# Kernel tuning notes

Hardware: AMD Instinct MI355X
Metric: run time of the kernel (lower is better)

The kernel has to match this reference:

```python
import jax, jax.numpy as jnp
import numpy as np

NPOINT = 1024
BRANCHES = [(0.4, 32), (0.8, 64)]  # (radius, nsample)
SPECS = [[67, 64, 64, 128], [67, 64, 128, 256]]  # mlp specs after use_xyz (+3)
EPS = 1e-5


def setup_inputs() -> dict:
    key = jax.random.key(0)
    ks = jax.random.split(key, 16)
    B, N, C = 8, 8192, 64
    inp = {
        "xyz": jax.random.normal(ks[0], (B, N, 3), jnp.float32),
        "features": jax.random.normal(ks[1], (B, C, N), jnp.float32),
    }
    ki = 2
    for bi, spec in enumerate(SPECS):
        for li in range(3):
            o, i = spec[li + 1], spec[li]
            inp[f"w{bi}_{li}"] = jax.random.normal(ks[ki], (o, i), jnp.float32) * (1.0 / np.sqrt(i)); ki += 1
            inp[f"g{bi}_{li}"] = jnp.ones((o,), jnp.float32)
            inp[f"b{bi}_{li}"] = jnp.zeros((o,), jnp.float32)
    return inp


def fps(pts, npoint):
    # pts: [B, N+1, 3] (mean point prepended); sequential farthest point sampling
    B, N1, _ = pts.shape

    def step(carry, _):
        dist, far = carry
        idx3 = jnp.broadcast_to(far[:, None, None], (B, 1, 3))
        centroid = jnp.take_along_axis(pts, idx3, axis=1)  # [B,1,3]
        d = jnp.sum((pts - centroid) ** 2, axis=-1)        # [B,N+1]
        dist = jnp.minimum(dist, d)
        far2 = jnp.argmax(dist, axis=-1)
        return (dist, far2), centroid[:, 0, :]

    dist0 = jnp.full((B, N1), 1e10, jnp.float32)
    far0 = jnp.zeros((B,), jnp.int32)
    _, locs = jax.lax.scan(step, (dist0, far0), None, length=npoint)
    return jnp.transpose(locs, (1, 0, 2))  # [B, npoint, 3]


def ball_query(xyz, new_xyz, radius, nsample):
    # first <=nsample indices with dist^2 < radius^2, padded with first valid (0 if none)
    B, N, _ = xyz.shape
    d2 = jnp.sum((new_xyz[:, :, None, :] - xyz[:, None, :, :]) ** 2, axis=-1)  # [B,S,N]
    score = jnp.where(d2 < radius * radius, jnp.arange(N, dtype=jnp.int32), N)
    vals, _ = jax.lax.top_k(-score, nsample)  # smallest scores = earliest valid indices
    idx = -vals                               # [B,S,nsample], N marks invalid
    first = idx[..., :1]
    first = jnp.where(first < N, first, 0)
    return jnp.where(idx < N, idx, first)


def _forward(xyz, features, params):
    mean = jnp.mean(xyz, axis=1, keepdims=True)
    pts = jnp.concatenate([mean, xyz], axis=1)          # prepend mean point
    new_xyz = jax.lax.stop_gradient(fps(pts, NPOINT))   # [B,npoint,3] (torch no_grad)
    outs = []
    for (radius, nsample), layers in zip(BRANCHES, params):
        idx = ball_query(xyz, new_xyz, radius, nsample)           # [B,S,K]
        gxyz = jax.vmap(lambda p, i: p[i])(xyz, idx)              # [B,S,K,3]
        rel = jnp.transpose(gxyz - new_xyz[:, :, None, :], (0, 3, 1, 2))  # [B,3,S,K]
        gfeat = jax.vmap(lambda f, i: f[:, i])(features, idx)     # [B,C,S,K]
        x = jnp.concatenate([rel, gfeat], axis=1)                 # [B,3+C,S,K]
        for W, g, b in layers:  # Conv2d 1x1 (no bias) + BatchNorm (train stats) + ReLU
            x = jnp.einsum('oi,bisk->bosk', W, x)
            m = jnp.mean(x, axis=(0, 2, 3), keepdims=True)
            v = jnp.var(x, axis=(0, 2, 3), keepdims=True)
            x = (x - m) / jnp.sqrt(v + EPS) * g[None, :, None, None] + b[None, :, None, None]
            x = jax.nn.relu(x)
        outs.append(jnp.max(x, axis=3))                           # [B,Cout,S]
    return new_xyz, jnp.concatenate(outs, axis=1)


def reference(xyz, features,
              w0_0, g0_0, b0_0, w0_1, g0_1, b0_1, w0_2, g0_2, b0_2,
              w1_0, g1_0, b1_0, w1_1, g1_1, b1_1, w1_2, g1_2, b1_2):
    params = [
        [(w0_0, g0_0, b0_0), (w0_1, g0_1, b0_1), (w0_2, g0_2, b0_2)],
        [(w1_0, g1_0, b1_0), (w1_1, g1_1, b1_1), (w1_2, g1_2, b1_2)],
    ]
    return _forward(xyz, features, params)
```

## Files before the change

kernel.cpp:

```cpp
#include <hip/hip_runtime.h>
#include <hip/hip_bf16.h>
#include <cstdint>


typedef __attribute__((ext_vector_type(8))) short short8;
typedef __attribute__((ext_vector_type(4))) float f32x4;
typedef __attribute__((ext_vector_type(2))) float f32x2;

__device__ __forceinline__ float bf2f(unsigned short u) {
    return __uint_as_float(((unsigned)u) << 16);
}
__device__ __forceinline__ unsigned short f2bf(float f) {
    unsigned u = __float_as_uint(f);
    return (unsigned short)((u + 0x7fffu + ((u >> 16) & 1u)) >> 16);
}

__device__ __forceinline__ float wave_red_max_f32(float v) {
#define DPPSTEP(ctrl)                                                                  \
    {                                                                                  \
        int _t = __builtin_amdgcn_update_dpp((int)0xFF800000, __float_as_int(v), ctrl, \
                                             0xf, 0xf, false);                         \
        v = fmaxf(v, __int_as_float(_t));                                              \
    }
    DPPSTEP(0x111) DPPSTEP(0x112) DPPSTEP(0x114) DPPSTEP(0x118) DPPSTEP(0x142) DPPSTEP(0x143)
#undef DPPSTEP
    return v;
}
__device__ __forceinline__ unsigned wave_red_min_u32(unsigned v) {
#define DPPSTEP(ctrl)                                                                   \
    {                                                                                   \
        unsigned _t = (unsigned)__builtin_amdgcn_update_dpp((int)0xFFFFFFFF, (int)v,    \
                                                            ctrl, 0xf, 0xf, false);     \
        v = v < _t ? v : _t;                                                            \
    }
    DPPSTEP(0x111) DPPSTEP(0x112) DPPSTEP(0x114) DPPSTEP(0x118) DPPSTEP(0x142) DPPSTEP(0x143)
#undef DPPSTEP
    return v;
}
__device__ __forceinline__ unsigned long long u64max(unsigned long long a, unsigned long long b) {
    return a > b ? a : b;
}
__device__ __forceinline__ unsigned u32min(unsigned a, unsigned b) { return a < b ? a : b; }

static const size_t OFF_WBF   = 0;
static const size_t OFF_STATS = 262144;
static const size_t STATS_BYTES = 720896;
static const size_t OFF_AFF   = 1048576;
static const size_t OFF_IDX0  = 2097152;
static const size_t OFF_IDX1  = 3145728;
static const size_t OFF_MX    = 5242880;
static const size_t OFF_MN    = 13631488;
static const size_t OFF_Y0    = 22020096;
static const size_t OFF_Y1    = 90177536;
static const size_t OFF_FEATT = 211812352;

__global__ __launch_bounds__(256) void fused_pre(
    const float* __restrict__ xyz, const float* __restrict__ feat,
    float* __restrict__ newxyz, unsigned short* __restrict__ ft,
    const float* __restrict__ w0, const float* __restrict__ w1, const float* __restrict__ w2,
    const float* __restrict__ w3, const float* __restrict__ w4, const float* __restrict__ w5,
    unsigned short* __restrict__ wb) {
    __shared__ union alignas(16) SM {
        struct {
            float ptsx[8200], ptsy[8200], ptsz[8200];
            float ldsM[16][3];
            float meanv[3];
            unsigned long long sKey[2][4];
            float cbuf[3072];
        } f;
        float tile[64][65];
    } sm;
    const int tid = threadIdx.x;

    if (blockIdx.x >= 1032) {
        int id = (int)(blockIdx.x - 1032) * 256 + tid;
        const int psz[6] = {6144, 4096, 8192, 6144, 8192, 32768};
        const int Kp[6] = {96, 64, 64, 96, 64, 128};
        const int Ks[6] = {67, 64, 64, 67, 64, 128};
        const float* wp[6] = {w0, w1, w2, w3, w4, w5};
        int off = 0;
        for (int l = 0; l < 6; ++l) {
            if (id < off + psz[l]) {
                int e = id - off;
                int m = e / Kp[l], k = e - m * Kp[l];
                float v = (k < Ks[l]) ? wp[l][m * Ks[l] + k] : 0.f;
                wb[id] = f2bf(v);
                return;
            }
            off += psz[l];
        }
        return;
    }

    if (blockIdx.x >= 8) {
        int tb = (int)blockIdx.x - 8;
        int b = tb >> 7;
        int j0 = (tb & 127) * 64;
#pragma unroll
        for (int i = 0; i < 16; ++i) {
            int e = i * 256 + tid;
            int c = e >> 6, j = e & 63;
            sm.tile[j][c] = feat[((size_t)b * 64 + c) * 8192 + j0 + j];
        }
        __syncthreads();
#pragma unroll
        for (int i = 0; i < 16; ++i) {
            int e = i * 256 + tid;
            int j = e >> 6, c = e & 63;
            ft[((size_t)(b * 8192 + j0 + j)) * 96 + 3 + c] = f2bf(sm.tile[j][c]);
        }
        if (tid < 64) {
            int j = tid;
            size_t base = ((size_t)(b * 8192 + j0 + j)) * 96;
            const float* xp = xyz + ((size_t)b * 8192 + j0 + j) * 3;
            ft[base + 0] = f2bf(xp[0]);
            ft[base + 1] = f2bf(xp[1]);
            ft[base + 2] = f2bf(xp[2]);
        } else if (tid < 128) {
            int j = tid - 64;
            size_t base = ((size_t)(b * 8192 + j0 + j)) * 96;
            for (int c = 67; c < 96; ++c) ft[base + c] = 0;
        }
        return;
    }

    const int b = blockIdx.x;
    const int t = tid;
    const int lane = t & 63, wv = t >> 6;
    const float* xb = xyz + (size_t)b * 8192 * 3;

    f32x2 px[16], py[16], pz[16], d[16];
#pragma unroll
    for (int k = 0; k < 16; ++k) {
        int q0 = t + 256 * (2 * k);
        int q1 = t + 256 * (2 * k + 1);
        px[k].x = xb[q0 * 3 + 0]; px[k].y = xb[q1 * 3 + 0];
        py[k].x = xb[q0 * 3 + 1]; py[k].y = xb[q1 * 3 + 1];
        pz[k].x = xb[q0 * 3 + 2]; pz[k].y = xb[q1 * 3 + 2];
        d[k].x = 1e10f; d[k].y = 1e10f;
        sm.f.ptsx[q0 + 1] = px[k].x; sm.f.ptsx[q1 + 1] = px[k].y;
        sm.f.ptsy[q0 + 1] = py[k].x; sm.f.ptsy[q1 + 1] = py[k].y;
        sm.f.ptsz[q0 + 1] = pz[k].x; sm.f.ptsz[q1 + 1] = pz[k].y;
    }
    {
        float sx[4], sy[4], sz[4];
#pragma unroll
        for (int m = 0; m < 4; ++m) {
            int u = (t + 256 * m + 1023) & 1023;
            float ax = 0.f, ay = 0.f, az = 0.f;
#pragma unroll
            for (int jj = 0; jj < 8; ++jj) {
                int ia = u + 1024 * jj;
                ax += xb[ia * 3 + 0]; ay += xb[ia * 3 + 1]; az += xb[ia * 3 + 2];
            }
            sx[m] = ax; sy[m] = ay; sz[m] = az;
        }
#pragma unroll
        for (int off = 32; off; off >>= 1) {
#pragma unroll
            for (int m = 0; m < 4; ++m) {
                sx[m] += __shfl_xor(sx[m], off, 64);
                sy[m] += __shfl_xor(sy[m], off, 64);
                sz[m] += __shfl_xor(sz[m], off, 64);
            }
        }
        if (lane == 0) {
#pragma unroll
            for (int m = 0; m < 4; ++m) {
                sm.f.ldsM[wv + 4 * m][0] = sx[m];
                sm.f.ldsM[wv + 4 * m][1] = sy[m];
                sm.f.ldsM[wv + 4 * m][2] = sz[m];
            }
        }
    }
    __syncthreads();
    if (t < 3) {
        float s = 0.f;
        for (int w = 0; w < 16; ++w) s += sm.f.ldsM[w][t];
        sm.f.meanv[t] = s * (1.f / 8192.f);
    }
    __syncthreads();
    float cx = sm.f.meanv[0], cy = sm.f.meanv[1], cz = sm.f.meanv[2];
    const float mmx = cx, mmy = cy, mmz = cz;
    float dm = 1e10f;
    if (t == 0) { sm.f.ptsx[0] = cx; sm.f.ptsy[0] = cy; sm.f.ptsz[0] = cz; }
    __syncthreads();

    for (int it = 0; it < 1024; ++it) {
        if (t == 0) {
            sm.f.cbuf[it * 3 + 0] = cx;
            sm.f.cbuf[it * 3 + 1] = cy;
            sm.f.cbuf[it * 3 + 2] = cz;
        }
        f32x2 c0, c1, c2, vm2;
        c0.x = cx; c0.y = cx; c1.x = cy; c1.y = cy; c2.x = cz; c2.y = cz;
        vm2.x = -1e30f; vm2.y = -1e30f;
        {
#pragma clang fp contract(off)
#pragma unroll
            for (int k = 0; k < 16; ++k) {
                f32x2 dx = px[k] - c0;
                f32x2 dy = py[k] - c1;
                f32x2 dz = pz[k] - c2;
                f32x2 dd = (dx * dx + dy * dy) + dz * dz;
                f32x2 nd = __builtin_elementwise_min(d[k], dd);
                d[k] = nd;
                vm2 = __builtin_elementwise_max(vm2, nd);
            }
        }
        float vmax = fmaxf(vm2.x, vm2.y);
        if (t == 0) {
            float dx = __fsub_rn(mmx, cx);
            float dy = __fsub_rn(mmy, cy);
            float dz = __fsub_rn(mmz, cz);
            float dd = __fadd_rn(__fadd_rn(__fmul_rn(dx, dx), __fmul_rn(dy, dy)), __fmul_rn(dz, dz));
            dm = fminf(dm, dd);
            vmax = fmaxf(vmax, dm);
        }
        float wm = wave_red_max_f32(vmax);
        float bmaxw = __int_as_float(__builtin_amdgcn_readlane(__float_as_int(wm), 63));
        unsigned m2[16];
#pragma unroll
        for (int k = 0; k < 16; ++k) {
            unsigned i0 = (d[k].x == bmaxw) ? (unsigned)(t + 256 * (2 * k) + 1) : 0xFFFFFFFFu;
            unsigned i1 = (d[k].y == bmaxw) ? (unsigned)(t + 256 * (2 * k + 1) + 1) : 0xFFFFFFFFu;
            m2[k] = u32min(i0, i1);
        }
#pragma unroll
        for (int s = 8; s; s >>= 1)
#pragma unroll
            for (int k = 0; k < s; ++k) m2[k] = u32min(m2[k], m2[k + s]);
        unsigned mi = m2[0];
        if (t == 0 && dm == bmaxw) mi = 0u;
        unsigned wmin = wave_red_min_u32(mi);
        unsigned miw = (unsigned)__builtin_amdgcn_readlane((int)wmin, 63);
        int par = it & 1;
        if (lane == 0)
            sm.f.sKey[par][wv] = ((unsigned long long)__float_as_uint(bmaxw) << 32) |
                                 (unsigned long long)(8192u - miw);
        __syncthreads();
        unsigned long long ka[4];
#pragma unroll
        for (int i = 0; i < 4; ++i) ka[i] = sm.f.sKey[par][i];
        unsigned long long kk = u64max(u64max(ka[0], ka[1]), u64max(ka[2], ka[3]));
        int far = 8192 - (int)(unsigned)(kk & 0xffffffffull);
        cx = sm.f.ptsx[far];
        cy = sm.f.ptsy[far];
        cz = sm.f.ptsz[far];
    }
    __syncthreads();
    float* ob = newxyz + (size_t)b * 3072;
#pragma unroll
    for (int i = 0; i < 12; ++i) ob[t + 256 * i] = sm.f.cbuf[t + 256 * i];
}

__global__ void ball_query2(const float* __restrict__ xyz, const float* __restrict__ newxyz,
                            int* __restrict__ idx0, int* __restrict__ idx1) {
    int bid = blockIdx.x;
    int br = (bid >= 2048);
    int K = br ? 64 : 32;
    float r2 = br ? (0.8f * 0.8f) : (0.4f * 0.4f);
    int* idxout = br ? idx1 : idx0;
    int wid = (((bid & 2047) * 256) + threadIdx.x) >> 6;
    int lane = threadIdx.x & 63;
    int b = wid >> 10;
    const float* q = newxyz + (size_t)wid * 3;
    float qx = q[0], qy = q[1], qz = q[2];
    const float* xb = xyz + (size_t)b * 8192 * 3;
    int* out = idxout + (size_t)wid * K;
    int count = 0;
    int first = 0;
    for (int base = 0; base < 8192 && count < K; base += 64) {
        int j = base + lane;
        float dx = __fsub_rn(xb[j * 3 + 0], qx);
        float dy = __fsub_rn(xb[j * 3 + 1], qy);
        float dz = __fsub_rn(xb[j * 3 + 2], qz);
        float d2 = __fadd_rn(__fadd_rn(__fmul_rn(dx, dx), __fmul_rn(dy, dy)), __fmul_rn(dz, dz));
        bool in = d2 < r2;
        unsigned long long m = __ballot(in);
        if (count == 0 && m) first = base + __ffsll((long long)m) - 1;
        if (in) {
            int pos = count + __popcll(m & ((1ull << lane) - 1ull));
            if (pos < K) out[pos] = j;
        }
        count += __popcll(m);
    }
    if (count < K) {
        int fillv = (count > 0) ? first : 0;
        for (int p = count + lane; p < K; p += 64) out[p] = fillv;
    }
}

template <int Mp, int Kp, int IN_MODE, int OUT_MODE, int KSH, int NT>
__global__ __launch_bounds__(256) void gemm_mfma(
    const unsigned short* __restrict__ Wb, const unsigned short* __restrict__ Xin,
    const float* __restrict__ aff, const int* __restrict__ idx,
    const unsigned short* __restrict__ ftp, const float* __restrict__ newxyz,
    unsigned short* __restrict__ Yout, float* __restrict__ MX, float* __restrict__ MN,
    float* __restrict__ statS, float* __restrict__ statQ) {
    constexpr int MT = Mp / 64;
    constexpr int KS = Kp / 32;
    constexpr int NC = NT * 16;
    constexpr int NCHUNK = NT * KS * 64;
    __shared__ unsigned short Bs[NCHUNK * 8];
    __shared__ float sAux[NT * 64];
    int* sAuxI = (int*)sAux;

    const int tid = threadIdx.x;
    const int w = tid >> 6;
    const int lane = tid & 63;
    const int n = lane & 15;
    const int quad = lane >> 4;
    const int rbase = w * (Mp / 4);
    const long col0 = (long)blockIdx.x * NC;

    short8 a[MT][KS];
#pragma unroll
    for (int mt = 0; mt < MT; ++mt)
#pragma unroll
        for (int ks = 0; ks < KS; ++ks)
            a[mt][ks] = *(const short8*)(Wb + (size_t)(rbase + mt * 16 + n) * Kp + ks * 32 + quad * 8);

    if constexpr (IN_MODE == 0) {
        for (int c = tid; c < NC; c += 256) {
            long colg = col0 + c;
            sAuxI[c] = idx[colg];
            long sk = colg >> KSH;
            sAux[NC + c] = newxyz[sk * 3 + 0];
            sAux[2 * NC + c] = newxyz[sk * 3 + 1];
            sAux[3 * NC + c] = newxyz[sk * 3 + 2];
        }
    } else {
        if (tid < 2 * Kp) sAux[tid] = aff[tid];
    }
    __syncthreads();

#pragma unroll
    for (int i = 0; i < NCHUNK / 256; ++i) {
        int p = i * 256 + tid;
        int pl = p & 63;
        int pn = pl & 15;
        int pq = pl >> 4;
        int rest = p >> 6;
        int pks = rest % KS;
        int pnt = rest / KS;
        int col = pnt * 16 + pn;
        int kc = pks * 4 + pq;
        short8 v;
        if constexpr (IN_MODE == 0) {
            const int bb = (int)(col0 >> (KSH + 10));
            int j = sAuxI[col];
            v = *(const short8*)(ftp + ((long)(bb * 8192 + j)) * 96 + kc * 8);
            if (kc == 0) {
                v[0] = (short)f2bf(bf2f((unsigned short)v[0]) - sAux[NC + col]);
                v[1] = (short)f2bf(bf2f((unsigned short)v[1]) - sAux[2 * NC + col]);
                v[2] = (short)f2bf(bf2f((unsigned short)v[2]) - sAux[3 * NC + col]);
            }
        } else {
            short8 raw = *(const short8*)(Xin + (col0 + col) * (long)Kp + kc * 8);
#pragma unroll
            for (int e = 0; e < 8; ++e) {
                float xf = bf2f((unsigned short)raw[e]);
                xf = fmaxf(fmaf(xf, sAux[kc * 8 + e], sAux[Kp + kc * 8 + e]), 0.f);
                v[e] = (short)f2bf(xf);
            }
        }
        *(short8*)(&Bs[p * 8]) = v;
    }
    __syncthreads();

    f32x4 acc[MT][NT];
#pragma unroll
    for (int mt = 0; mt < MT; ++mt)
#pragma unroll
        for (int nt = 0; nt < NT; ++nt)
#pragma unroll
            for (int r = 0; r < 4; ++r) acc[mt][nt][r] = 0.f;

#pragma unroll
    for (int ks = 0; ks < KS; ++ks) {
#pragma unroll
        for (int nt = 0; nt < NT; ++nt) {
            short8 bfr = *(const short8*)(&Bs[((nt * KS + ks) * 64 + lane) * 8]);
#pragma unroll
            for (int mt = 0; mt < MT; ++mt)
                acc[mt][nt] = __builtin_amdgcn_mfma_f32_16x16x32_bf16(a[mt][ks], bfr, acc[mt][nt], 0, 0, 0);
        }
    }

    const int slot = (int)(blockIdx.x & 127);
#pragma unroll
    for (int mt = 0; mt < MT; ++mt)
#pragma unroll
        for (int r = 0; r < 4; ++r) {
            float s = 0.f, q = 0.f;
#pragma unroll
            for (int nt = 0; nt < NT; ++nt) {
                float v = acc[mt][nt][r];
                s += v;
                q = fmaf(v, v, q);
            }
#pragma unroll
            for (int off = 1; off < 16; off <<= 1) {
                s += __shfl_xor(s, off, 16);
                q += __shfl_xor(q, off, 16);
            }
            if (n == 0) {
                int ch = rbase + mt * 16 + quad * 4 + r;
                atomicAdd(statS + (size_t)ch * 128 + slot, s);
                atomicAdd(statQ + (size_t)ch * 128 + slot, q);
            }
        }

    if constexpr (OUT_MODE == 0) {
#pragma unroll
        for (int mt = 0; mt < MT; ++mt)
#pragma unroll
            for (int nt = 0; nt < NT; ++nt) {
                long col = col0 + nt * 16 + n;
                unsigned p0 = f2bf(acc[mt][nt][0]) | ((unsigned)f2bf(acc[mt][nt][1]) << 16);
                unsigned p1 = f2bf(acc[mt][nt][2]) | ((unsigned)f2bf(acc[mt][nt][3]) << 16);
                uint2 st; st.x = p0; st.y = p1;
                *(uint2*)(Yout + col * Mp + rbase + mt * 16 + quad * 4) = st;
            }
    } else {
        constexpr int GRP = (1 << KSH) / 16;
        constexpr int NG = NT / GRP;
#pragma unroll
        for (int mt = 0; mt < MT; ++mt)
#pragma unroll
            for (int r = 0; r < 4; ++r) {
#pragma unroll
                for (int gh = 0; gh < NG; ++gh) {
                    float mx = acc[mt][GRP * gh][r], mn = acc[mt][GRP * gh][r];
#pragma unroll
                    for (int e = 1; e < GRP; ++e) {
                        mx = fmaxf(mx, acc[mt][GRP * gh + e][r]);
                        mn = fminf(mn, acc[mt][GRP * gh + e][r]);
                    }
#pragma unroll
                    for (int off = 1; off < 16; off <<= 1) {
                        mx = fmaxf(mx, __shfl_xor(mx, off, 16));
                        mn = fminf(mn, __shfl_xor(mn, off, 16));
                    }
                    if (n == 0) {
                        int ch = rbase + mt * 16 + quad * 4 + r;
                        long g = (col0 >> KSH) + gh;
                        MX[(long)ch * 8192 + g] = mx;
                        MN[(long)ch * 8192 + g] = mn;
                    }
                }
            }
    }
}

__global__ void finalize_kernel(const float* __restrict__ sS, const float* __restrict__ sQ,
                                const float* __restrict__ g, const float* __restrict__ b,
                                float* __restrict__ aff, int C, float invCount) {
    int c = threadIdx.x + blockIdx.x * blockDim.x;
    if (c >= C) return;
    float s = 0.f, q = 0.f;
    for (int k = 0; k < 128; ++k) { s += sS[c * 128 + k]; q += sQ[c * 128 + k]; }
    float mean = s * invCount;
    float var = fmaxf(q * invCount - mean * mean, 0.f);
    float sc = g[c] / sqrtf(var + 1e-5f);
    float sh = b[c] - mean * sc;
    aff[c] = sc;
    aff[C + c] = sh;
}

__global__ void final_out_kernel(const float* __restrict__ MX, const float* __restrict__ MN,
                                 const float* __restrict__ aff, float* __restrict__ out1,
                                 int Cout, int cOff) {
    long i = (long)blockIdx.x * 256 + threadIdx.x;
    int c = (int)(i >> 13);
    int gidx = (int)(i & 8191);
    int b = gidx >> 10, s = gidx & 1023;
    float sc = aff[c], sh = aff[Cout + c];
    float v = fmaxf(fmaxf(sc * MX[i] + sh, sc * MN[i] + sh), 0.f);
    out1[((long)b * 384 + cOff + c) * 1024 + s] = v;
}

extern "C" void kernel_launch(void* const* d_in, const int* in_sizes, int n_in,
                              void* d_out, int out_size, void* d_ws, size_t ws_size,
                              hipStream_t stream) {
    const float* xyz = (const float*)d_in[0];
    const float* feat = (const float*)d_in[1];
    const float *W[6], *G[6], *Bi[6];
    for (int l = 0; l < 6; ++l) {
        W[l] = (const float*)d_in[2 + l * 3];
        G[l] = (const float*)d_in[3 + l * 3];
        Bi[l] = (const float*)d_in[4 + l * 3];
    }
    char* ws = (char*)d_ws;
    float* out0 = (float*)d_out;
    float* out1 = (float*)d_out + 24576;

    unsigned short* wb = (unsigned short*)(ws + OFF_WBF);
    float* stats = (float*)(ws + OFF_STATS);
    float* affine = (float*)(ws + OFF_AFF);
    int* idx0 = (int*)(ws + OFF_IDX0);
    int* idx1 = (int*)(ws + OFF_IDX1);
    float* mx = (float*)(ws + OFF_MX);
    float* mn = (float*)(ws + OFF_MN);
    unsigned short* y0 = (unsigned short*)(ws + OFF_Y0);
    unsigned short* y1 = (unsigned short*)(ws + OFF_Y1);
    unsigned short* ftp = (unsigned short*)(ws + OFF_FEATT);

    hipMemsetAsync(stats, 0, STATS_BYTES, stream);
    fused_pre<<<1288, 256, 0, stream>>>(xyz, feat, out0, ftp, W[0], W[1], W[2], W[3], W[4],
                                        W[5], wb);
    ball_query2<<<4096, 256, 0, stream>>>(xyz, out0, idx0, idx1);

    const int wOff[6] = {0, 6144, 10240, 18432, 24576, 32768};
    int stOff[6], afOff[6];
    {
        const int Cs[6] = {64, 64, 128, 64, 128, 256};
        int so = 0, ao = 0;
        for (int l = 0; l < 6; ++l) {
            stOff[l] = so; so += Cs[l] * 256;
            afOff[l] = ao; ao += Cs[l] * 2;
        }
    }

    for (int br = 0; br < 2; ++br) {
        const int K = br ? 64 : 32;
        const long NCOL = 8L * 1024 * K;
        int* idx = br ? idx1 : idx0;
        const int l0 = br * 3, l1 = br * 3 + 1, l2 = br * 3 + 2;
        const int M2 = br ? 256 : 128;
        const float invCount = 1.f / (float)NCOL;
        const int nblk256 = (int)(NCOL / 256);
        const int nblk128 = (int)(NCOL / 128);
        const int nblk64 = (int)(NCOL / 64);

        if (br == 0) {
            gemm_mfma<64, 96, 0, 0, 5, 16><<<nblk256, 256, 0, stream>>>(
                wb + wOff[l0], nullptr, nullptr, idx, ftp, out0, y0, nullptr, nullptr,
                stats + stOff[l0], stats + stOff[l0] + 64 * 128);
            finalize_kernel<<<1, 256, 0, stream>>>(stats + stOff[l0], stats + stOff[l0] + 64 * 128,
                                                   G[l0], Bi[l0], affine + afOff[l0], 64, invCount);
            gemm_mfma<64, 64, 1, 0, 5, 16><<<nblk256, 256, 0, stream>>>(
                wb + wOff[l1], y0, affine + afOff[l0], nullptr, nullptr, nullptr, y1, nullptr,
                nullptr, stats + stOff[l1], stats + stOff[l1] + 64 * 128);
            finalize_kernel<<<1, 256, 0, stream>>>(stats + stOff[l1], stats + stOff[l1] + 64 * 128,
                                                   G[l1], Bi[l1], affine + afOff[l1], 64, invCount);
            gemm_mfma<128, 64, 1, 1, 5, 8><<<nblk128, 256, 0, stream>>>(
                wb + wOff[l2], y1, affine + afOff[l1], nullptr, nullptr, nullptr, nullptr, mx, mn,
                stats + stOff[l2], stats + stOff[l2] + 128 * 128);
            finalize_kernel<<<1, 256, 0, stream>>>(stats + stOff[l2], stats + stOff[l2] + 128 * 128,
                                                   G[l2], Bi[l2], affine + afOff[l2], 128, invCount);
        } else {
            gemm_mfma<64, 96, 0, 0, 6, 16><<<nblk256, 256, 0, stream>>>(
                wb + wOff[l0], nullptr, nullptr, idx, ftp, out0, y0, nullptr, nullptr,
                stats + stOff[l0], stats + stOff[l0] + 64 * 128);
            finalize_kernel<<<1, 256, 0, stream>>>(stats + stOff[l0], stats + stOff[l0] + 64 * 128,
                                                   G[l0], Bi[l0], affine + afOff[l0], 64, invCount);
            gemm_mfma<128, 64, 1, 0, 6, 8><<<nblk128, 256, 0, stream>>>(
                wb + wOff[l1], y0, affine + afOff[l0], nullptr, nullptr, nullptr, y1, nullptr,
                nullptr, stats + stOff[l1], stats + stOff[l1] + 128 * 128);
            finalize_kernel<<<1, 256, 0, stream>>>(stats + stOff[l1], stats + stOff[l1] + 128 * 128,
                                                   G[l1], Bi[l1], affine + afOff[l1], 128, invCount);
            gemm_mfma<256, 128, 1, 1, 6, 4><<<nblk64, 256, 0, stream>>>(
                wb + wOff[l2], y1, affine + afOff[l1], nullptr, nullptr, nullptr, nullptr, mx, mn,
                stats + stOff[l2], stats + stOff[l2] + 256 * 128);
            finalize_kernel<<<1, 256, 0, stream>>>(stats + stOff[l2], stats + stOff[l2] + 256 * 128,
                                                   G[l2], Bi[l2], affine + afOff[l2], 256, invCount);
        }

        final_out_kernel<<<(M2 * 8192) / 256, 256, 0, stream>>>(mx, mn, affine + afOff[l2], out1,
                                                                M2, br ? 128 : 0);
    }
}
```

Baseline: 1.635 ms.

## Merge independent branch GEMM stages into shared launches to overlap work

```diff
diff --git a/kernel.cpp b/kernel.cpp
--- a/kernel.cpp
+++ b/kernel.cpp
@@ -292,7 +292,8 @@
 }
 
 template <int Mp, int Kp, int IN_MODE, int OUT_MODE, int KSH, int NT>
-__global__ __launch_bounds__(256) void gemm_mfma(
+__device__ __forceinline__ void gemm_body(
+    int bid, char* smemRaw,
     const unsigned short* __restrict__ Wb, const unsigned short* __restrict__ Xin,
     const float* __restrict__ aff, const int* __restrict__ idx,
     const unsigned short* __restrict__ ftp, const float* __restrict__ newxyz,
@@ -302,8 +303,8 @@
     constexpr int KS = Kp / 32;
     constexpr int NC = NT * 16;
     constexpr int NCHUNK = NT * KS * 64;
-    __shared__ unsigned short Bs[NCHUNK * 8];
-    __shared__ float sAux[NT * 64];
+    unsigned short* Bs = (unsigned short*)smemRaw;
+    float* sAux = (float*)(smemRaw + (size_t)NCHUNK * 16);
     int* sAuxI = (int*)sAux;
 
     const int tid = threadIdx.x;
@@ -312,7 +313,7 @@
     const int n = lane & 15;
     const int quad = lane >> 4;
     const int rbase = w * (Mp / 4);
-    const long col0 = (long)blockIdx.x * NC;
+    const long col0 = (long)bid * NC;
 
     short8 a[MT][KS];
 #pragma unroll
@@ -388,7 +389,7 @@
         }
     }
 
-    const int slot = (int)(blockIdx.x & 127);
+    const int slot = bid & 127;
 #pragma unroll
     for (int mt = 0; mt < MT; ++mt)
 #pragma unroll
@@ -451,6 +452,57 @@
                     }
                 }
             }
+    }
+}
+
+template <int Mp, int Kp, int IN_MODE, int OUT_MODE, int KSH, int NT>
+__global__ __launch_bounds__(256) void gemm_mfma(
+    const unsigned short* __restrict__ Wb, const unsigned short* __restrict__ Xin,
+    const float* __restrict__ aff, const int* __restrict__ idx,
+    const unsigned short* __restrict__ ftp, const float* __restrict__ newxyz,
+    unsigned short* __restrict__ Yout, float* __restrict__ MX, float* __restrict__ MN,
+    float* __restrict__ statS, float* __restrict__ statQ) {
+    constexpr int SMEM = NT * (Kp / 32) * 64 * 16 + NT * 64 * 4;
+    __shared__ alignas(16) char smem[SMEM];
+    gemm_body<Mp, Kp, IN_MODE, OUT_MODE, KSH, NT>(blockIdx.x, smem, Wb, Xin, aff, idx, ftp,
+                                                  newxyz, Yout, MX, MN, statS, statQ);
+}
+
+__global__ __launch_bounds__(256) void gemm_l2b0_l0b1(
+    const unsigned short* __restrict__ WbA, const unsigned short* __restrict__ XinA,
+    const float* __restrict__ affA, float* __restrict__ MXA, float* __restrict__ MNA,
+    float* __restrict__ sSA, float* __restrict__ sQA,
+    const unsigned short* __restrict__ WbB, const int* __restrict__ idxB,
+    const unsigned short* __restrict__ ftpB, const float* __restrict__ newxyzB,
+    unsigned short* __restrict__ YoutB, float* __restrict__ sSB, float* __restrict__ sQB,
+    int nA) {
+    extern __shared__ char smem[];
+    if ((int)blockIdx.x < nA)
+        gemm_body<128, 64, 1, 1, 5, 8>((int)blockIdx.x, smem, WbA, XinA, affA, nullptr, nullptr,
+                                       nullptr, nullptr, MXA, MNA, sSA, sQA);
+    else
+        gemm_body<64, 96, 0, 0, 6, 16>((int)blockIdx.x - nA, smem, WbB, nullptr, nullptr, idxB,
+                                       ftpB, newxyzB, YoutB, nullptr, nullptr, sSB, sQB);
+}
+
+__global__ __launch_bounds__(256) void gemm_l1b1_fo0(
+    const unsigned short* __restrict__ Wb, const unsigned short* __restrict__ Xin,
+    const float* __restrict__ aff, unsigned short* __restrict__ Yout,
+    float* __restrict__ sS, float* __restrict__ sQ,
+    const float* __restrict__ MX, const float* __restrict__ MN,
+    const float* __restrict__ affF, float* __restrict__ out1, int nA) {
+    extern __shared__ char smem[];
+    if ((int)blockIdx.x < nA) {
+        gemm_body<128, 64, 1, 0, 6, 8>((int)blockIdx.x, smem, Wb, Xin, aff, nullptr, nullptr,
+                                       nullptr, Yout, nullptr, nullptr, sS, sQ);
+    } else {
+        long i = (long)((int)blockIdx.x - nA) * 256 + threadIdx.x;
+        int c = (int)(i >> 13);
+        int gidx = (int)(i & 8191);
+        int b = gidx >> 10, s = gidx & 1023;
+        float sc = affF[c], sh = affF[128 + c];
+        float v = fmaxf(fmaxf(sc * MX[i] + sh, sc * MN[i] + sh), 0.f);
+        out1[((long)b * 384 + c) * 1024 + s] = v;
     }
 }
 
@@ -469,6 +521,31 @@
     aff[C + c] = sh;
 }
 
+__global__ void finalize2_kernel(const float* __restrict__ sS0, const float* __restrict__ sQ0,
+                                 const float* __restrict__ g0, const float* __restrict__ b0,
+                                 float* __restrict__ aff0, int C0, float ic0,
+                                 const float* __restrict__ sS1, const float* __restrict__ sQ1,
+                                 const float* __restrict__ g1, const float* __restrict__ b1,
+                                 float* __restrict__ aff1, int C1, float ic1) {
+    const float* sS = blockIdx.x ? sS1 : sS0;
+    const float* sQ = blockIdx.x ? sQ1 : sQ0;
+    const float* g = blockIdx.x ? g1 : g0;
+    const float* b = blockIdx.x ? b1 : b0;
+    float* aff = blockIdx.x ? aff1 : aff0;
+    int C = blockIdx.x ? C1 : C0;
+    float ic = blockIdx.x ? ic1 : ic0;
+    int c = threadIdx.x;
+    if (c >= C) return;
+    float s = 0.f, q = 0.f;
+    for (int k = 0; k < 128; ++k) { s += sS[c * 128 + k]; q += sQ[c * 128 + k]; }
+    float mean = s * ic;
+    float var = fmaxf(q * ic - mean * mean, 0.f);
+    float sc = g[c] / sqrtf(var + 1e-5f);
+    float sh = b[c] - mean * sc;
+    aff[c] = sc;
+    aff[C + c] = sh;
+}
+
 __global__ void final_out_kernel(const float* __restrict__ MX, const float* __restrict__ MN,
                                  const float* __restrict__ aff, float* __restrict__ out1,
                                  int Cout, int cOff) {
@@ -522,53 +599,39 @@
             afOff[l] = ao; ao += Cs[l] * 2;
         }
     }
-
-    for (int br = 0; br < 2; ++br) {
-        const int K = br ? 64 : 32;
-        const long NCOL = 8L * 1024 * K;
-        int* idx = br ? idx1 : idx0;
-        const int l0 = br * 3, l1 = br * 3 + 1, l2 = br * 3 + 2;
-        const int M2 = br ? 256 : 128;
-        const float invCount = 1.f / (float)NCOL;
-        const int nblk256 = (int)(NCOL / 256);
-        const int nblk128 = (int)(NCOL / 128);
-        const int nblk64 = (int)(NCOL / 64);
-
-        if (br == 0) {
-            gemm_mfma<64, 96, 0, 0, 5, 16><<<nblk256, 256, 0, stream>>>(
-                wb + wOff[l0], nullptr, nullptr, idx, ftp, out0, y0, nullptr, nullptr,
-                stats + stOff[l0], stats + stOff[l0] + 64 * 128);
-            finalize_kernel<<<1, 256, 0, stream>>>(stats + stOff[l0], stats + stOff[l0] + 64 * 128,
-                                                   G[l0], Bi[l0], affine + afOff[l0], 64, invCount);
-            gemm_mfma<64, 64, 1, 0, 5, 16><<<nblk256, 256, 0, stream>>>(
-                wb + wOff[l1], y0, affine + afOff[l0], nullptr, nullptr, nullptr, y1, nullptr,
-                nullptr, stats + stOff[l1], stats + stOff[l1] + 64 * 128);
-            finalize_kernel<<<1, 256, 0, stream>>>(stats + stOff[l1], stats + stOff[l1] + 64 * 128,
-                                                   G[l1], Bi[l1], affine + afOff[l1], 64, invCount);
-            gemm_mfma<128, 64, 1, 1, 5, 8><<<nblk128, 256, 0, stream>>>(
-                wb + wOff[l2], y1, affine + afOff[l1], nullptr, nullptr, nullptr, nullptr, mx, mn,
-                stats + stOff[l2], stats + stOff[l2] + 128 * 128);
-            finalize_kernel<<<1, 256, 0, stream>>>(stats + stOff[l2], stats + stOff[l2] + 128 * 128,
-                                                   G[l2], Bi[l2], affine + afOff[l2], 128, invCount);
-        } else {
-            gemm_mfma<64, 96, 0, 0, 6, 16><<<nblk256, 256, 0, stream>>>(
-                wb + wOff[l0], nullptr, nullptr, idx, ftp, out0, y0, nullptr, nullptr,
-                stats + stOff[l0], stats + stOff[l0] + 64 * 128);
-            finalize_kernel<<<1, 256, 0, stream>>>(stats + stOff[l0], stats + stOff[l0] + 64 * 128,
-                                                   G[l0], Bi[l0], affine + afOff[l0], 64, invCount);
-            gemm_mfma<128, 64, 1, 0, 6, 8><<<nblk128, 256, 0, stream>>>(
-                wb + wOff[l1], y0, affine + afOff[l0], nullptr, nullptr, nullptr, y1, nullptr,
-                nullptr, stats + stOff[l1], stats + stOff[l1] + 128 * 128);
-            finalize_kernel<<<1, 256, 0, stream>>>(stats + stOff[l1], stats + stOff[l1] + 128 * 128,
-                                                   G[l1], Bi[l1], affine + afOff[l1], 128, invCount);
-            gemm_mfma<256, 128, 1, 1, 6, 4><<<nblk64, 256, 0, stream>>>(
-                wb + wOff[l2], y1, affine + afOff[l1], nullptr, nullptr, nullptr, nullptr, mx, mn,
-                stats + stOff[l2], stats + stOff[l2] + 256 * 128);
-            finalize_kernel<<<1, 256, 0, stream>>>(stats + stOff[l2], stats + stOff[l2] + 256 * 128,
-                                                   G[l2], Bi[l2], affine + afOff[l2], 256, invCount);
-        }
-
-        final_out_kernel<<<(M2 * 8192) / 256, 256, 0, stream>>>(mx, mn, affine + afOff[l2], out1,
-                                                                M2, br ? 128 : 0);
-    }
-}
+    const float ic0 = 1.f / (float)(8L * 1024 * 32);
+    const float ic1 = 1.f / (float)(8L * 1024 * 64);
+
+    gemm_mfma<64, 96, 0, 0, 5, 16><<<1024, 256, 0, stream>>>(
+        wb + wOff[0], nullptr, nullptr, idx0, ftp, out0, y0, nullptr, nullptr,
+        stats + stOff[0], stats + stOff[0] + 64 * 128);
+    finalize_kernel<<<1, 256, 0, stream>>>(stats + stOff[0], stats + stOff[0] + 64 * 128,
+                                           G[0], Bi[0], affine + afOff[0], 64, ic0);
+    gemm_mfma<64, 64, 1, 0, 5, 16><<<1024, 256, 0, stream>>>(
+        wb + wOff[1], y0, affine + afOff[0], nullptr, nullptr, nullptr, y1, nullptr,
+        nullptr, stats + stOff[1], stats + stOff[1] + 64 * 128);
+    finalize_kernel<<<1, 256, 0, stream>>>(stats + stOff[1], stats + stOff[1] + 64 * 128,
+                                           G[1], Bi[1], affine + afOff[1], 64, ic0);
+
+    gemm_l2b0_l0b1<<<4096, 256, 53248, stream>>>(
+        wb + wOff[2], y1, affine + afOff[1], mx, mn, stats + stOff[2],
+        stats + stOff[2] + 128 * 128, wb + wOff[3], idx1, ftp, out0, y0, stats + stOff[3],
+        stats + stOff[3] + 64 * 128, 2048);
+    finalize2_kernel<<<2, 256, 0, stream>>>(
+        stats + stOff[2], stats + stOff[2] + 128 * 128, G[2], Bi[2], affine + afOff[2], 128, ic0,
+        stats + stOff[3], stats + stOff[3] + 64 * 128, G[3], Bi[3], affine + afOff[3], 64, ic1);
+
+    gemm_l1b1_fo0<<<8192, 256, 18432, stream>>>(
+        wb + wOff[4], y0, affine + afOff[3], y1, stats + stOff[4], stats + stOff[4] + 128 * 128,
+        mx, mn, affine + afOff[2], out1, 4096);
+    finalize_kernel<<<1, 256, 0, stream>>>(stats + stOff[4], stats + stOff[4] + 128 * 128,
+                                           G[4], Bi[4], affine + afOff[4], 128, ic1);
+
+    gemm_mfma<256, 128, 1, 1, 6, 4><<<8192, 256, 0, stream>>>(
+        wb + wOff[5], y1, affine + afOff[4], nullptr, nullptr, nullptr, nullptr, mx, mn,
+        stats + stOff[5], stats + stOff[5] + 256 * 128);
+    finalize_kernel<<<1, 256, 0, stream>>>(stats + stOff[5], stats + stOff[5] + 256 * 128,
+                                           G[5], Bi[5], affine + afOff[5], 256, ic1);
+    final_out_kernel<<<(256 * 8192) / 256, 256, 0, stream>>>(mx, mn, affine + afOff[5], out1,
+                                                             256, 128);
+}
```

Measured after the change: 1.636 ms. Within noise of the previous version (+0.0%).
